# Kernel optimization log

Hardware: AMD Instinct MI355X
Metric: run time of the kernel (lower is better)

## Reference

```python
import jax, jax.numpy as jnp
import numpy as np

D_MODEL = 2048
N_EXPERTS = 64
TOP_K = 8
N_TOKENS = 16384


def setup_inputs() -> dict:
    key = jax.random.key(0)
    k1, k2 = jax.random.split(key)
    x_flat = jax.random.normal(k1, (N_TOKENS, D_MODEL), dtype=jnp.float32)
    # nn.Linear(d_model, n_experts) weight has shape [n_experts, d_model]
    gate_w = jax.random.normal(k2, (N_EXPERTS, D_MODEL), dtype=jnp.float32) * (1.0 / np.sqrt(D_MODEL))
    return {"x_flat": x_flat, "gate_w": gate_w}


def reference(x_flat, gate_w):
    # logits = x_flat @ gate_w.T : [tokens, n_experts]
    logits = jnp.einsum("td,ed->te", x_flat, gate_w)
    full_probs = jax.nn.softmax(logits, axis=-1)
    topk_logits, topk_idx = jax.lax.top_k(logits, TOP_K)
    topk_weights = jax.nn.softmax(topk_logits, axis=-1)
    return topk_idx, topk_weights, full_probs, logits
```

## Files before the change

### kernel.cpp

```cpp
#include <hip/hip_runtime.h>
#include <math.h>

#define D_MODEL   2048
#define N_EXPERTS 64
#define TOP_K     8
#define N_TOKENS  16384
#define TOK_TILE  64
#define NTHREADS  512
#define WS_NEED   (64*4*3*64*16)

typedef __attribute__((ext_vector_type(8))) short bf16x8;
typedef __attribute__((ext_vector_type(4))) float f32x4;
typedef __attribute__((ext_vector_type(4))) int   i32x4;

union FragU { i32x4 i; bf16x8 h; };

__device__ __forceinline__ void split3(float x, unsigned &h, unsigned &m, unsigned &l) {
    unsigned ux = __float_as_uint(x);
    h = ux & 0xffff0000u;
    float mf = x - __uint_as_float(h);
    unsigned um = __float_as_uint(mf) & 0xffff0000u;
    float lf = mf - __uint_as_float(um);
    m = um;
    l = __float_as_uint(lf) & 0xffff0000u;
}

__global__ __launch_bounds__(256) void pack_w_kernel(const float* __restrict__ gw,
                                                     unsigned* __restrict__ wp) {
    const int g    = blockIdx.x * 256 + threadIdx.x;
    const int d    = g & 3;
    const int lane = (g >> 2) & 63;
    const int rest = g >> 8;
    const int v    = rest % 3;
    const int t    = rest / 3;
    const int fr   = t & 3;
    const int ks   = t >> 2;
    const int e    = fr * 16 + (lane & 15);
    const int k    = ks * 32 + (lane >> 4) * 8 + 2 * d;
    const float w0 = gw[(size_t)e * D_MODEL + k];
    const float w1 = gw[(size_t)e * D_MODEL + k + 1];
    unsigned h0, m0, l0, h1, m1, l1;
    split3(w0, h0, m0, l0);
    split3(w1, h1, m1, l1);
    const unsigned c0 = (v == 0) ? h0 : ((v == 1) ? m0 : l0);
    const unsigned c1 = (v == 0) ? h1 : ((v == 1) ? m1 : l1);
    wp[g] = (c0 >> 16) | c1;
}

__device__ __forceinline__ void splitpack(const float4 a, const float4 b,
                                          FragU &ph, FragU &pm, FragU &pl) {
    const float f[8] = {a.x, a.y, a.z, a.w, b.x, b.y, b.z, b.w};
#pragma unroll
    for (int d = 0; d < 4; ++d) {
        unsigned h0, m0, l0, h1, m1, l1;
        split3(f[2 * d],     h0, m0, l0);
        split3(f[2 * d + 1], h1, m1, l1);
        ph.i[d] = (int)((h0 >> 16) | h1);
        pm.i[d] = (int)((m0 >> 16) | m1);
        pl.i[d] = (int)((l0 >> 16) | l1);
    }
}

#define MFMA(A_, B_, C_) C_ = __builtin_amdgcn_mfma_f32_16x16x32_bf16((A_).h, (B_).h, C_, 0, 0, 0)

__global__ __launch_bounds__(NTHREADS) void router_mfma(
    const float* __restrict__ x, const unsigned* __restrict__ wp,
    float* __restrict__ out)
{
    __shared__ float lt[TOK_TILE][N_EXPERTS + 1];
    __shared__ float smax[TOK_TILE], srs[TOK_TILE];

    const int tid  = threadIdx.x;
    const int lane = tid & 63;
    const int wv   = tid >> 6;
    const int mrow = wv & 1;
    const int ncol = (wv >> 1) & 1;
    const int kh   = wv >> 2;
    const int m0   = blockIdx.x * TOK_TILE;

    const int lrow = lane & 15;
    const int lk   = lane >> 4;

    const float* xr0 = x + (size_t)(m0 + mrow * 32 + lrow) * D_MODEL + lk * 8;
    const float* xr1 = xr0 + (size_t)16 * D_MODEL;

    f32x4 acc00 = {0.f, 0.f, 0.f, 0.f};
    f32x4 acc01 = acc00, acc10 = acc00, acc11 = acc00;

    const unsigned* wb = wp + (size_t)(ncol * 2 * 3) * 256 + lane * 4;

    int ks = kh;
    float4 A0a = *(const float4*)(xr0 + ks * 32);
    float4 A0b = *(const float4*)(xr0 + ks * 32 + 4);
    float4 A1a = *(const float4*)(xr1 + ks * 32);
    float4 A1b = *(const float4*)(xr1 + ks * 32 + 4);
    const unsigned* bt = wb + ks * 3072;
    i32x4 B0h = *(const i32x4*)(bt +    0);
    i32x4 B0m = *(const i32x4*)(bt +  256);
    i32x4 B0l = *(const i32x4*)(bt +  512);
    i32x4 B1h = *(const i32x4*)(bt +  768);
    i32x4 B1m = *(const i32x4*)(bt + 1024);
    i32x4 B1l = *(const i32x4*)(bt + 1280);

    auto compute = [&](float4 cA0a, float4 cA0b, float4 cA1a, float4 cA1b,
                       i32x4 cB0h, i32x4 cB0m, i32x4 cB0l,
                       i32x4 cB1h, i32x4 cB1m, i32x4 cB1l) {
        FragU a0h, a0m, a0l, a1h, a1m, a1l;
        splitpack(cA0a, cA0b, a0h, a0m, a0l);
        splitpack(cA1a, cA1b, a1h, a1m, a1l);
        FragU b0h, b0m, b0l, b1h, b1m, b1l;
        b0h.i = cB0h; b0m.i = cB0m; b0l.i = cB0l;
        b1h.i = cB1h; b1m.i = cB1m; b1l.i = cB1l;
        MFMA(a0h, b0h, acc00); MFMA(a0h, b0m, acc00); MFMA(a0m, b0h, acc00);
        MFMA(a0h, b0l, acc00); MFMA(a0l, b0h, acc00); MFMA(a0m, b0m, acc00);
        MFMA(a0h, b1h, acc01); MFMA(a0h, b1m, acc01); MFMA(a0m, b1h, acc01);
        MFMA(a0h, b1l, acc01); MFMA(a0l, b1h, acc01); MFMA(a0m, b1m, acc01);
        MFMA(a1h, b0h, acc10); MFMA(a1h, b0m, acc10); MFMA(a1m, b0h, acc10);
        MFMA(a1h, b0l, acc10); MFMA(a1l, b0h, acc10); MFMA(a1m, b0m, acc10);
        MFMA(a1h, b1h, acc11); MFMA(a1h, b1m, acc11); MFMA(a1m, b1h, acc11);
        MFMA(a1h, b1l, acc11); MFMA(a1l, b1h, acc11); MFMA(a1m, b1m, acc11);
    };

    for (int t = 0; t < 31; ++t) {
        const int ks2 = ks + 2;
        float4 N0a = *(const float4*)(xr0 + ks2 * 32);
        float4 N0b = *(const float4*)(xr0 + ks2 * 32 + 4);
        float4 N1a = *(const float4*)(xr1 + ks2 * 32);
        float4 N1b = *(const float4*)(xr1 + ks2 * 32 + 4);
        const unsigned* bt2 = wb + ks2 * 3072;
        i32x4 C0h = *(const i32x4*)(bt2 +    0);
        i32x4 C0m = *(const i32x4*)(bt2 +  256);
        i32x4 C0l = *(const i32x4*)(bt2 +  512);
        i32x4 C1h = *(const i32x4*)(bt2 +  768);
        i32x4 C1m = *(const i32x4*)(bt2 + 1024);
        i32x4 C1l = *(const i32x4*)(bt2 + 1280);

        compute(A0a, A0b, A1a, A1b, B0h, B0m, B0l, B1h, B1m, B1l);

        A0a = N0a; A0b = N0b; A1a = N1a; A1b = N1b;
        B0h = C0h; B0m = C0m; B0l = C0l; B1h = C1h; B1m = C1m; B1l = C1l;
        ks = ks2;
    }
    compute(A0a, A0b, A1a, A1b, B0h, B0m, B0l, B1h, B1m, B1l);

    if (kh == 1) {
#pragma unroll
        for (int r = 0; r < 4; ++r) {
            lt[mrow * 32 +  0 + lk * 4 + r][ncol * 32 +  0 + lrow] = acc00[r];
            lt[mrow * 32 +  0 + lk * 4 + r][ncol * 32 + 16 + lrow] = acc01[r];
            lt[mrow * 32 + 16 + lk * 4 + r][ncol * 32 +  0 + lrow] = acc10[r];
            lt[mrow * 32 + 16 + lk * 4 + r][ncol * 32 + 16 + lrow] = acc11[r];
        }
    }
    __syncthreads();
    if (kh == 0) {
#pragma unroll
        for (int r = 0; r < 4; ++r) {
            lt[mrow * 32 +  0 + lk * 4 + r][ncol * 32 +  0 + lrow] += acc00[r];
            lt[mrow * 32 +  0 + lk * 4 + r][ncol * 32 + 16 + lrow] += acc01[r];
            lt[mrow * 32 + 16 + lk * 4 + r][ncol * 32 +  0 + lrow] += acc10[r];
            lt[mrow * 32 + 16 + lk * 4 + r][ncol * 32 + 16 + lrow] += acc11[r];
        }
    }
    __syncthreads();

    float* out_idx = out;
    float* out_w   = out + (size_t)N_TOKENS * TOP_K;
    float* out_p   = out + (size_t)2 * N_TOKENS * TOP_K;
    float* out_l   = out_p + (size_t)N_TOKENS * N_EXPERTS;

    if (tid < TOK_TILE) {
        const int t = tid;
        float tv[TOP_K];
        int   ti[TOP_K];
#pragma unroll
        for (int i = 0; i < TOP_K; ++i) { tv[i] = -INFINITY; ti[i] = 0; }
        float m = -INFINITY;

        for (int e = 0; e < N_EXPERTS; ++e) {
            const float v = lt[t][e];
            m = fmaxf(m, v);
            if (v > tv[TOP_K - 1]) {
#pragma unroll
                for (int j = TOP_K - 1; j >= 1; --j) {
                    const bool shift = (v > tv[j - 1]);
                    const bool here  = (v > tv[j]);
                    const float ntv = shift ? tv[j - 1] : (here ? v : tv[j]);
                    const int   nti = shift ? ti[j - 1] : (here ? e : ti[j]);
                    tv[j] = ntv; ti[j] = nti;
                }
                if (v > tv[0]) { tv[0] = v; ti[0] = e; }
            }
        }

        float s = 0.f;
        for (int e = 0; e < N_EXPERTS; ++e) s += expf(lt[t][e] - m);
        const float rs = 1.f / s;
        smax[t] = m;
        srs[t]  = rs;

        float ex[TOP_K];
        float wsum = 0.f;
#pragma unroll
        for (int i = 0; i < TOP_K; ++i) { ex[i] = expf(tv[i] - tv[0]); wsum += ex[i]; }
        const float rw = 1.f / wsum;

        const int tok = m0 + t;
#pragma unroll
        for (int i = 0; i < TOP_K; ++i) {
            out_idx[(size_t)tok * TOP_K + i] = (float)ti[i];
            out_w  [(size_t)tok * TOP_K + i] = ex[i] * rw;
        }
    }
    __syncthreads();

#pragma unroll
    for (int rep = 0; rep < 2; ++rep) {
        const int f = rep * (NTHREADS * 4) + tid * 4;
        const int t = f >> 6;
        const int e = f & 63;
        const float l0 = lt[t][e + 0];
        const float l1 = lt[t][e + 1];
        const float l2 = lt[t][e + 2];
        const float l3 = lt[t][e + 3];
        const float mm = smax[t];
        const float rr = srs[t];
        float4 pv = make_float4(expf(l0 - mm) * rr, expf(l1 - mm) * rr,
                                expf(l2 - mm) * rr, expf(l3 - mm) * rr);
        float4 lv = make_float4(l0, l1, l2, l3);
        const size_t gbase = (size_t)m0 * N_EXPERTS + f;
        *(float4*)(out_p + gbase) = pv;
        *(float4*)(out_l + gbase) = lv;
    }
}

__global__ __launch_bounds__(NTHREADS) void router_fallback(
    const float* __restrict__ x, const float* __restrict__ gw,
    float* __restrict__ out)
{
    __shared__ float xs[TOK_TILE][33];
    __shared__ float wsh[N_EXPERTS][36];
    __shared__ float lt[TOK_TILE][N_EXPERTS + 1];
    __shared__ float smax[TOK_TILE], srs[TOK_TILE];

    const int tid  = threadIdx.x;
    const int lane = tid & 63;
    const int wv   = tid >> 6;
    const int m0   = blockIdx.x * TOK_TILE;
    const int srow = tid >> 3;
    const int skq  = (tid & 7) * 4;

    const float* xsrc = x  + (size_t)(m0 + srow) * D_MODEL + skq;
    const float* wsrc = gw + (size_t)srow        * D_MODEL + skq;
    float4 xr = *(const float4*)(xsrc);
    float4 wr = *(const float4*)(wsrc);

    float acc[8];
#pragma unroll
    for (int i = 0; i < 8; ++i) acc[i] = 0.f;
    const int e0 = wv * 8;

    for (int c = 0; c < D_MODEL / 32; ++c) {
        xs[srow][skq] = xr.x; xs[srow][skq+1] = xr.y; xs[srow][skq+2] = xr.z; xs[srow][skq+3] = xr.w;
        *(float4*)&wsh[srow][skq] = wr;
        __syncthreads();
        if (c + 1 < D_MODEL / 32) {
            xr = *(const float4*)(xsrc + (c + 1) * 32);
            wr = *(const float4*)(wsrc + (c + 1) * 32);
        }
#pragma unroll 8
        for (int k4 = 0; k4 < 8; ++k4) {
            const float4 xv = *(const float4*)&xs[lane][k4 * 4];
#pragma unroll
            for (int e = 0; e < 8; ++e) {
                const float4 w4 = *(const float4*)&wsh[e0 + e][k4 * 4];
                acc[e] = fmaf(xv.x, w4.x, fmaf(xv.y, w4.y, fmaf(xv.z, w4.z, fmaf(xv.w, w4.w, acc[e]))));
            }
        }
        __syncthreads();
    }
#pragma unroll
    for (int e = 0; e < 8; ++e) lt[lane][e0 + e] = acc[e];
    __syncthreads();

    float* out_idx = out;
    float* out_w   = out + (size_t)N_TOKENS * TOP_K;
    float* out_p   = out + (size_t)2 * N_TOKENS * TOP_K;
    float* out_l   = out_p + (size_t)N_TOKENS * N_EXPERTS;

    if (tid < TOK_TILE) {
        const int t = tid;
        float tv[TOP_K]; int ti[TOP_K];
#pragma unroll
        for (int i = 0; i < TOP_K; ++i) { tv[i] = -INFINITY; ti[i] = 0; }
        float m = -INFINITY;
        for (int e = 0; e < N_EXPERTS; ++e) {
            const float v = lt[t][e];
            m = fmaxf(m, v);
            if (v > tv[TOP_K - 1]) {
#pragma unroll
                for (int j = TOP_K - 1; j >= 1; --j) {
                    const bool shift = (v > tv[j - 1]);
                    const bool here  = (v > tv[j]);
                    const float ntv = shift ? tv[j - 1] : (here ? v : tv[j]);
                    const int   nti = shift ? ti[j - 1] : (here ? e : ti[j]);
                    tv[j] = ntv; ti[j] = nti;
                }
                if (v > tv[0]) { tv[0] = v; ti[0] = e; }
            }
        }
        float s = 0.f;
        for (int e = 0; e < N_EXPERTS; ++e) s += expf(lt[t][e] - m);
        const float rs = 1.f / s;
        smax[t] = m; srs[t] = rs;
        float ex[TOP_K]; float wsum = 0.f;
#pragma unroll
        for (int i = 0; i < TOP_K; ++i) { ex[i] = expf(tv[i] - tv[0]); wsum += ex[i]; }
        const float rw = 1.f / wsum;
        const int tok = m0 + t;
#pragma unroll
        for (int i = 0; i < TOP_K; ++i) {
            out_idx[(size_t)tok * TOP_K + i] = (float)ti[i];
            out_w  [(size_t)tok * TOP_K + i] = ex[i] * rw;
        }
    }
    __syncthreads();
#pragma unroll
    for (int rep = 0; rep < 2; ++rep) {
        const int f = rep * (NTHREADS * 4) + tid * 4;
        const int t = f >> 6;
        const int e = f & 63;
        const float l0 = lt[t][e], l1 = lt[t][e+1], l2 = lt[t][e+2], l3 = lt[t][e+3];
        const float mm = smax[t], rr = srs[t];
        float4 pv = make_float4(expf(l0-mm)*rr, expf(l1-mm)*rr, expf(l2-mm)*rr, expf(l3-mm)*rr);
        float4 lv = make_float4(l0, l1, l2, l3);
        const size_t gbase = (size_t)m0 * N_EXPERTS + f;
        *(float4*)(out_p + gbase) = pv;
        *(float4*)(out_l + gbase) = lv;
    }
}

extern "C" void kernel_launch(void* const* d_in, const int* in_sizes, int n_in,
                              void* d_out, int out_size, void* d_ws, size_t ws_size,
                              hipStream_t stream) {
    const float* x  = (const float*)d_in[0];
    const float* gw = (const float*)d_in[1];
    float* out = (float*)d_out;
    if (ws_size >= (size_t)WS_NEED) {
        unsigned* wp = (unsigned*)d_ws;
        pack_w_kernel<<<dim3(WS_NEED / 4 / 256), dim3(256), 0, stream>>>(gw, wp);
        router_mfma<<<dim3(N_TOKENS / TOK_TILE), dim3(NTHREADS), 0, stream>>>(x, wp, out);
    } else {
        router_fallback<<<dim3(N_TOKENS / TOK_TILE), dim3(NTHREADS), 0, stream>>>(x, gw, out);
    }
}
```

Measured before the change: 74.79 us.

## Stage x tiles in swizzled LDS with double buffering, drop K-split across waves

```diff
diff --git a/kernel.cpp b/kernel.cpp
--- a/kernel.cpp
+++ b/kernel.cpp
@@ -67,100 +67,86 @@
     const float* __restrict__ x, const unsigned* __restrict__ wp,
     float* __restrict__ out)
 {
+    __shared__ __align__(16) float xs[2][TOK_TILE][64];
     __shared__ float lt[TOK_TILE][N_EXPERTS + 1];
     __shared__ float smax[TOK_TILE], srs[TOK_TILE];
 
     const int tid  = threadIdx.x;
     const int lane = tid & 63;
     const int wv   = tid >> 6;
-    const int mrow = wv & 1;
-    const int ncol = (wv >> 1) & 1;
-    const int kh   = wv >> 2;
+    const int mrow = wv & 3;
+    const int ncol = wv >> 2;
     const int m0   = blockIdx.x * TOK_TILE;
 
     const int lrow = lane & 15;
     const int lk   = lane >> 4;
 
-    const float* xr0 = x + (size_t)(m0 + mrow * 32 + lrow) * D_MODEL + lk * 8;
-    const float* xr1 = xr0 + (size_t)16 * D_MODEL;
-
-    f32x4 acc00 = {0.f, 0.f, 0.f, 0.f};
-    f32x4 acc01 = acc00, acc10 = acc00, acc11 = acc00;
-
-    const unsigned* wb = wp + (size_t)(ncol * 2 * 3) * 256 + lane * 4;
-
-    int ks = kh;
-    float4 A0a = *(const float4*)(xr0 + ks * 32);
-    float4 A0b = *(const float4*)(xr0 + ks * 32 + 4);
-    float4 A1a = *(const float4*)(xr1 + ks * 32);
-    float4 A1b = *(const float4*)(xr1 + ks * 32 + 4);
-    const unsigned* bt = wb + ks * 3072;
-    i32x4 B0h = *(const i32x4*)(bt +    0);
-    i32x4 B0m = *(const i32x4*)(bt +  256);
-    i32x4 B0l = *(const i32x4*)(bt +  512);
-    i32x4 B1h = *(const i32x4*)(bt +  768);
-    i32x4 B1m = *(const i32x4*)(bt + 1024);
-    i32x4 B1l = *(const i32x4*)(bt + 1280);
-
-    auto compute = [&](float4 cA0a, float4 cA0b, float4 cA1a, float4 cA1b,
-                       i32x4 cB0h, i32x4 cB0m, i32x4 cB0l,
-                       i32x4 cB1h, i32x4 cB1m, i32x4 cB1l) {
-        FragU a0h, a0m, a0l, a1h, a1m, a1l;
-        splitpack(cA0a, cA0b, a0h, a0m, a0l);
-        splitpack(cA1a, cA1b, a1h, a1m, a1l);
-        FragU b0h, b0m, b0l, b1h, b1m, b1l;
-        b0h.i = cB0h; b0m.i = cB0m; b0l.i = cB0l;
-        b1h.i = cB1h; b1m.i = cB1m; b1l.i = cB1l;
-        MFMA(a0h, b0h, acc00); MFMA(a0h, b0m, acc00); MFMA(a0m, b0h, acc00);
-        MFMA(a0h, b0l, acc00); MFMA(a0l, b0h, acc00); MFMA(a0m, b0m, acc00);
-        MFMA(a0h, b1h, acc01); MFMA(a0h, b1m, acc01); MFMA(a0m, b1h, acc01);
-        MFMA(a0h, b1l, acc01); MFMA(a0l, b1h, acc01); MFMA(a0m, b1m, acc01);
-        MFMA(a1h, b0h, acc10); MFMA(a1h, b0m, acc10); MFMA(a1m, b0h, acc10);
-        MFMA(a1h, b0l, acc10); MFMA(a1l, b0h, acc10); MFMA(a1m, b0m, acc10);
-        MFMA(a1h, b1h, acc11); MFMA(a1h, b1m, acc11); MFMA(a1m, b1h, acc11);
-        MFMA(a1h, b1l, acc11); MFMA(a1l, b1h, acc11); MFMA(a1m, b1m, acc11);
-    };
-
-    for (int t = 0; t < 31; ++t) {
-        const int ks2 = ks + 2;
-        float4 N0a = *(const float4*)(xr0 + ks2 * 32);
-        float4 N0b = *(const float4*)(xr0 + ks2 * 32 + 4);
-        float4 N1a = *(const float4*)(xr1 + ks2 * 32);
-        float4 N1b = *(const float4*)(xr1 + ks2 * 32 + 4);
-        const unsigned* bt2 = wb + ks2 * 3072;
-        i32x4 C0h = *(const i32x4*)(bt2 +    0);
-        i32x4 C0m = *(const i32x4*)(bt2 +  256);
-        i32x4 C0l = *(const i32x4*)(bt2 +  512);
-        i32x4 C1h = *(const i32x4*)(bt2 +  768);
-        i32x4 C1m = *(const i32x4*)(bt2 + 1024);
-        i32x4 C1l = *(const i32x4*)(bt2 + 1280);
-
-        compute(A0a, A0b, A1a, A1b, B0h, B0m, B0l, B1h, B1m, B1l);
-
-        A0a = N0a; A0b = N0b; A1a = N1a; A1b = N1b;
-        B0h = C0h; B0m = C0m; B0l = C0l; B1h = C1h; B1m = C1m; B1l = C1l;
-        ks = ks2;
-    }
-    compute(A0a, A0b, A1a, A1b, B0h, B0m, B0l, B1h, B1m, B1l);
-
-    if (kh == 1) {
-#pragma unroll
-        for (int r = 0; r < 4; ++r) {
-            lt[mrow * 32 +  0 + lk * 4 + r][ncol * 32 +  0 + lrow] = acc00[r];
-            lt[mrow * 32 +  0 + lk * 4 + r][ncol * 32 + 16 + lrow] = acc01[r];
-            lt[mrow * 32 + 16 + lk * 4 + r][ncol * 32 +  0 + lrow] = acc10[r];
-            lt[mrow * 32 + 16 + lk * 4 + r][ncol * 32 + 16 + lrow] = acc11[r];
-        }
-    }
-    __syncthreads();
-    if (kh == 0) {
-#pragma unroll
-        for (int r = 0; r < 4; ++r) {
-            lt[mrow * 32 +  0 + lk * 4 + r][ncol * 32 +  0 + lrow] += acc00[r];
-            lt[mrow * 32 +  0 + lk * 4 + r][ncol * 32 + 16 + lrow] += acc01[r];
-            lt[mrow * 32 + 16 + lk * 4 + r][ncol * 32 +  0 + lrow] += acc10[r];
-            lt[mrow * 32 + 16 + lk * 4 + r][ncol * 32 + 16 + lrow] += acc11[r];
-        }
+    const int sr   = tid >> 3;
+    const int s0   = tid & 7;
+    const int wswz = (sr & 7) << 1;
+    float* dstA = &xs[0][sr][4 * (s0 ^ wswz)];
+    float* dstB = &xs[0][sr][4 * ((s0 ^ wswz) ^ 8)];
+    const float* xsrc = x + (size_t)(m0 + sr) * D_MODEL + 4 * s0;
+
+    float4 xa = *(const float4*)(xsrc);
+    float4 xb = *(const float4*)(xsrc + 32);
+    *(float4*)dstA = xa;
+    *(float4*)dstB = xb;
+
+    f32x4 acc0a = {0.f, 0.f, 0.f, 0.f};
+    f32x4 acc0b = acc0a, acc1a = acc0a, acc1b = acc0a;
+
+    const unsigned* wb = wp + (size_t)(ncol * 6) * 256 + lane * 4;
+    const int arow = mrow * 16 + lrow;
+    const int amsk = (lrow & 7) << 1;
+    const int LBUF = TOK_TILE * 64;
+    __syncthreads();
+
+    for (int c = 0; c < 32; ++c) {
+        if (c + 1 < 32) {
+            xa = *(const float4*)(xsrc + (c + 1) * 64);
+            xb = *(const float4*)(xsrc + (c + 1) * 64 + 32);
+        }
+        const float* xbuf = &xs[c & 1][0][0];
+#pragma unroll
+        for (int j = 0; j < 2; ++j) {
+            const int ks = 2 * c + j;
+            const unsigned* bt = wb + (size_t)ks * 3072;
+            i32x4 B0h = *(const i32x4*)(bt +    0);
+            i32x4 B0m = *(const i32x4*)(bt +  256);
+            i32x4 B0l = *(const i32x4*)(bt +  512);
+            i32x4 B1h = *(const i32x4*)(bt +  768);
+            i32x4 B1m = *(const i32x4*)(bt + 1024);
+            i32x4 B1l = *(const i32x4*)(bt + 1280);
+
+            const int slot = (j * 8 + 2 * lk) ^ amsk;
+            const float* ap = xbuf + arow * 64 + 4 * slot;
+            const float4 Aa = *(const float4*)(ap);
+            const float4 Ab = *(const float4*)(ap + 4);
+
+            FragU ah, am, al;
+            splitpack(Aa, Ab, ah, am, al);
+            FragU b0h, b0m, b0l, b1h, b1m, b1l;
+            b0h.i = B0h; b0m.i = B0m; b0l.i = B0l;
+            b1h.i = B1h; b1m.i = B1m; b1l.i = B1l;
+
+            MFMA(ah, b0h, acc0a); MFMA(am, b0h, acc0a); MFMA(al, b0h, acc0a);
+            MFMA(ah, b0m, acc0b); MFMA(am, b0m, acc0b); MFMA(ah, b0l, acc0b);
+            MFMA(ah, b1h, acc1a); MFMA(am, b1h, acc1a); MFMA(al, b1h, acc1a);
+            MFMA(ah, b1m, acc1b); MFMA(am, b1m, acc1b); MFMA(ah, b1l, acc1b);
+        }
+        if (c + 1 < 32) {
+            const int off = ((c + 1) & 1) * LBUF;
+            *(float4*)(dstA + off) = xa;
+            *(float4*)(dstB + off) = xb;
+        }
+        __syncthreads();
+    }
+
+#pragma unroll
+    for (int r = 0; r < 4; ++r) {
+        lt[mrow * 16 + lk * 4 + r][ncol * 32 +  0 + lrow] = acc0a[r] + acc0b[r];
+        lt[mrow * 16 + lk * 4 + r][ncol * 32 + 16 + lrow] = acc1a[r] + acc1b[r];
     }
     __syncthreads();
 
```

Measured after the change: 74.20 us. About the same (-0.8%).

## Split-K router GEMM across many blocks with separate reduce and top-k kernel

Applied to the files above, without the earlier changes.

```diff
diff --git a/kernel.cpp b/kernel.cpp
--- a/kernel.cpp
+++ b/kernel.cpp
@@ -5,9 +5,11 @@
 #define N_EXPERTS 64
 #define TOP_K     8
 #define N_TOKENS  16384
-#define TOK_TILE  64
-#define NTHREADS  512
-#define WS_NEED   (64*4*3*64*16)
+
+#define WS_PACK   786432u
+#define WS_PART   (8u*16384u*64u*4u)
+#define WS_NEED_BIG (WS_PACK + WS_PART)
+#define WS_NEED_MID WS_PACK
 
 typedef __attribute__((ext_vector_type(8))) short bf16x8;
 typedef __attribute__((ext_vector_type(4))) float f32x4;
@@ -63,12 +65,196 @@
 
 #define MFMA(A_, B_, C_) C_ = __builtin_amdgcn_mfma_f32_16x16x32_bf16((A_).h, (B_).h, C_, 0, 0, 0)
 
-__global__ __launch_bounds__(NTHREADS) void router_mfma(
+__global__ __launch_bounds__(512, 4) void gemm_ws(
+    const float* __restrict__ x, const unsigned* __restrict__ wp,
+    float* __restrict__ part)
+{
+    __shared__ __align__(16) float lds[2][64][68];
+
+    const int tid  = threadIdx.x;
+    const int lane = tid & 63;
+    const int w    = tid >> 6;
+    const int eg   = w & 3;
+    const int kg   = w >> 2;
+    const int bx   = blockIdx.x;
+    const int tc   = bx & 255;
+    const int kq   = bx >> 8;
+
+    const int lrow = lane & 15;
+    const int lk   = lane >> 4;
+
+    const int gk0 = kq * 8 + kg * 4;
+    const unsigned* wb = wp + lane * 4;
+#define WOFF(j, p) ((size_t)(((gk0 + (j)) * 4 + eg) * 3 + (p)) * 256)
+    const i32x4 W0h = *(const i32x4*)(wb + WOFF(0,0));
+    const i32x4 W0m = *(const i32x4*)(wb + WOFF(0,1));
+    const i32x4 W0l = *(const i32x4*)(wb + WOFF(0,2));
+    const i32x4 W1h = *(const i32x4*)(wb + WOFF(1,0));
+    const i32x4 W1m = *(const i32x4*)(wb + WOFF(1,1));
+    const i32x4 W1l = *(const i32x4*)(wb + WOFF(1,2));
+    const i32x4 W2h = *(const i32x4*)(wb + WOFF(2,0));
+    const i32x4 W2m = *(const i32x4*)(wb + WOFF(2,1));
+    const i32x4 W2l = *(const i32x4*)(wb + WOFF(2,2));
+    const i32x4 W3h = *(const i32x4*)(wb + WOFF(3,0));
+    const i32x4 W3m = *(const i32x4*)(wb + WOFF(3,1));
+    const i32x4 W3l = *(const i32x4*)(wb + WOFF(3,2));
+#undef WOFF
+
+    const float* pA = x + (size_t)(tc * 64 + lrow) * D_MODEL
+                      + kq * 256 + kg * 128 + lk * 8;
+
+    float4 Ca = *(const float4*)(pA);
+    float4 Cb = *(const float4*)(pA + 4);
+
+    for (int tile = 0; tile < 4; ++tile) {
+        f32x4 accA = {0.f, 0.f, 0.f, 0.f};
+        f32x4 accB = accA;
+
+#define KSTEP(j, WH, WM, WL)                                                 \
+        {                                                                    \
+            const int nt = ((j) < 3) ? tile : tile + 1;                      \
+            const int nj = ((j) + 1) & 3;                                    \
+            float4 Na = Ca, Nb = Cb;                                         \
+            if (!((tile) == 3 && (j) == 3)) {                                \
+                const float* pn = pA + (size_t)nt * 16 * D_MODEL + nj * 32;  \
+                Na = *(const float4*)(pn);                                   \
+                Nb = *(const float4*)(pn + 4);                               \
+            }                                                                \
+            FragU ah, am_, al;                                               \
+            splitpack(Ca, Cb, ah, am_, al);                                  \
+            FragU bh, bm, bl;                                                \
+            bh.i = WH; bm.i = WM; bl.i = WL;                                 \
+            MFMA(ah, bh, accA); MFMA(am_, bh, accA); MFMA(al, bh, accA);     \
+            MFMA(ah, bm, accB); MFMA(am_, bm, accB); MFMA(ah, bl, accB);     \
+            Ca = Na; Cb = Nb;                                                \
+        }
+        KSTEP(0, W0h, W0m, W0l)
+        KSTEP(1, W1h, W1m, W1l)
+        KSTEP(2, W2h, W2m, W2l)
+        KSTEP(3, W3h, W3m, W3l)
+#undef KSTEP
+
+#pragma unroll
+        for (int reg = 0; reg < 4; ++reg)
+            lds[kg][tile * 16 + lk * 4 + reg][eg * 16 + lrow]
+                = accA[reg] + accB[reg];
+    }
+    __syncthreads();
+
+    float* pout = part + (size_t)kq * N_TOKENS * 64 + (size_t)(tc * 64) * 64;
+#pragma unroll
+    for (int it = 0; it < 2; ++it) {
+        const int idx = it * 512 + tid;
+        const int tok = idx >> 4;
+        const int e4  = (idx & 15) * 4;
+        const float4 a = *(const float4*)&lds[0][tok][e4];
+        const float4 b = *(const float4*)&lds[1][tok][e4];
+        float4 r = make_float4(a.x + b.x, a.y + b.y, a.z + b.z, a.w + b.w);
+        *(float4*)(pout + (size_t)tok * 64 + e4) = r;
+    }
+}
+
+__global__ __launch_bounds__(256) void reduce_top(
+    const float* __restrict__ part, float* __restrict__ out)
+{
+    __shared__ float lt[16 * 68 + 32];
+    const int tid = threadIdx.x;
+    const int bx  = blockIdx.x;
+    const int m0  = bx * 16;
+
+    {
+        const int t16 = tid >> 4;
+        const int e4  = (tid & 15) * 4;
+        const size_t tok = (size_t)m0 + t16;
+        float4 s = {0.f, 0.f, 0.f, 0.f};
+#pragma unroll
+        for (int kq = 0; kq < 8; ++kq) {
+            const float4 v = *(const float4*)(part + (size_t)kq * N_TOKENS * 64
+                                              + tok * 64 + e4);
+            s.x += v.x; s.y += v.y; s.z += v.z; s.w += v.w;
+        }
+        *(float4*)(&lt[t16 * 68 + e4]) = s;
+    }
+    __syncthreads();
+
+    float* smax = lt + 16 * 68;
+    float* srs  = smax + 16;
+
+    float* out_idx = out;
+    float* out_w   = out + (size_t)N_TOKENS * TOP_K;
+    float* out_p   = out + (size_t)2 * N_TOKENS * TOP_K;
+    float* out_l   = out_p + (size_t)N_TOKENS * N_EXPERTS;
+
+    if (tid < 16) {
+        const int t = tid;
+        float tv[TOP_K];
+        int   ti[TOP_K];
+#pragma unroll
+        for (int i = 0; i < TOP_K; ++i) { tv[i] = -INFINITY; ti[i] = 0; }
+        float m = -INFINITY;
+
+        for (int e = 0; e < N_EXPERTS; ++e) {
+            const float v = lt[t * 68 + e];
+            m = fmaxf(m, v);
+            if (v > tv[TOP_K - 1]) {
+#pragma unroll
+                for (int j = TOP_K - 1; j >= 1; --j) {
+                    const bool shift = (v > tv[j - 1]);
+                    const bool here  = (v > tv[j]);
+                    const float ntv = shift ? tv[j - 1] : (here ? v : tv[j]);
+                    const int   nti = shift ? ti[j - 1] : (here ? e : ti[j]);
+                    tv[j] = ntv; ti[j] = nti;
+                }
+                if (v > tv[0]) { tv[0] = v; ti[0] = e; }
+            }
+        }
+
+        float s = 0.f;
+        for (int e = 0; e < N_EXPERTS; ++e) s += expf(lt[t * 68 + e] - m);
+        const float rs = 1.f / s;
+        smax[t] = m;
+        srs[t]  = rs;
+
+        float ex[TOP_K];
+        float wsum = 0.f;
+#pragma unroll
+        for (int i = 0; i < TOP_K; ++i) { ex[i] = expf(tv[i] - tv[0]); wsum += ex[i]; }
+        const float rw = 1.f / wsum;
+
+        const int tok = m0 + t;
+#pragma unroll
+        for (int i = 0; i < TOP_K; ++i) {
+            out_idx[(size_t)tok * TOP_K + i] = (float)ti[i];
+            out_w  [(size_t)tok * TOP_K + i] = ex[i] * rw;
+        }
+    }
+    __syncthreads();
+
+    {
+        const int f = tid * 4;
+        const int t = f >> 6;
+        const int e = f & 63;
+        const float l0 = lt[t * 68 + e + 0];
+        const float l1 = lt[t * 68 + e + 1];
+        const float l2 = lt[t * 68 + e + 2];
+        const float l3 = lt[t * 68 + e + 3];
+        const float mm = smax[t];
+        const float rr = srs[t];
+        float4 pv = make_float4(expf(l0 - mm) * rr, expf(l1 - mm) * rr,
+                                expf(l2 - mm) * rr, expf(l3 - mm) * rr);
+        float4 lv = make_float4(l0, l1, l2, l3);
+        const size_t gbase = (size_t)m0 * N_EXPERTS + f;
+        *(float4*)(out_p + gbase) = pv;
+        *(float4*)(out_l + gbase) = lv;
+    }
+}
+
+__global__ __launch_bounds__(512) void router_mfma_mid(
     const float* __restrict__ x, const unsigned* __restrict__ wp,
     float* __restrict__ out)
 {
-    __shared__ float lt[TOK_TILE][N_EXPERTS + 1];
-    __shared__ float smax[TOK_TILE], srs[TOK_TILE];
+    __shared__ float lt[64][N_EXPERTS + 1];
+    __shared__ float smax[64], srs[64];
 
     const int tid  = threadIdx.x;
     const int lane = tid & 63;
@@ -76,7 +262,7 @@
     const int mrow = wv & 1;
     const int ncol = (wv >> 1) & 1;
     const int kh   = wv >> 2;
-    const int m0   = blockIdx.x * TOK_TILE;
+    const int m0   = blockIdx.x * 64;
 
     const int lrow = lane & 15;
     const int lk   = lane >> 4;
@@ -169,14 +355,13 @@
     float* out_p   = out + (size_t)2 * N_TOKENS * TOP_K;
     float* out_l   = out_p + (size_t)N_TOKENS * N_EXPERTS;
 
-    if (tid < TOK_TILE) {
+    if (tid < 64) {
         const int t = tid;
         float tv[TOP_K];
         int   ti[TOP_K];
 #pragma unroll
         for (int i = 0; i < TOP_K; ++i) { tv[i] = -INFINITY; ti[i] = 0; }
         float m = -INFINITY;
-
         for (int e = 0; e < N_EXPERTS; ++e) {
             const float v = lt[t][e];
             m = fmaxf(m, v);
@@ -192,19 +377,14 @@
                 if (v > tv[0]) { tv[0] = v; ti[0] = e; }
             }
         }
-
         float s = 0.f;
         for (int e = 0; e < N_EXPERTS; ++e) s += expf(lt[t][e] - m);
         const float rs = 1.f / s;
-        smax[t] = m;
-        srs[t]  = rs;
-
-        float ex[TOP_K];
-        float wsum = 0.f;
+        smax[t] = m; srs[t] = rs;
+        float ex[TOP_K]; float wsum = 0.f;
 #pragma unroll
         for (int i = 0; i < TOP_K; ++i) { ex[i] = expf(tv[i] - tv[0]); wsum += ex[i]; }
         const float rw = 1.f / wsum;
-
         const int tok = m0 + t;
 #pragma unroll
         for (int i = 0; i < TOP_K; ++i) {
@@ -216,7 +396,7 @@
 
 #pragma unroll
     for (int rep = 0; rep < 2; ++rep) {
-        const int f = rep * (NTHREADS * 4) + tid * 4;
+        const int f = rep * (512 * 4) + tid * 4;
         const int t = f >> 6;
         const int e = f & 63;
         const float l0 = lt[t][e + 0];
@@ -234,19 +414,19 @@
     }
 }
 
-__global__ __launch_bounds__(NTHREADS) void router_fallback(
+__global__ __launch_bounds__(512) void router_fallback(
     const float* __restrict__ x, const float* __restrict__ gw,
     float* __restrict__ out)
 {
-    __shared__ float xs[TOK_TILE][33];
+    __shared__ float xs[64][33];
     __shared__ float wsh[N_EXPERTS][36];
-    __shared__ float lt[TOK_TILE][N_EXPERTS + 1];
-    __shared__ float smax[TOK_TILE], srs[TOK_TILE];
+    __shared__ float lt[64][N_EXPERTS + 1];
+    __shared__ float smax[64], srs[64];
 
     const int tid  = threadIdx.x;
     const int lane = tid & 63;
     const int wv   = tid >> 6;
-    const int m0   = blockIdx.x * TOK_TILE;
+    const int m0   = blockIdx.x * 64;
     const int srow = tid >> 3;
     const int skq  = (tid & 7) * 4;
 
@@ -288,7 +468,7 @@
     float* out_p   = out + (size_t)2 * N_TOKENS * TOP_K;
     float* out_l   = out_p + (size_t)N_TOKENS * N_EXPERTS;
 
-    if (tid < TOK_TILE) {
+    if (tid < 64) {
         const int t = tid;
         float tv[TOP_K]; int ti[TOP_K];
 #pragma unroll
@@ -327,7 +507,7 @@
     __syncthreads();
 #pragma unroll
     for (int rep = 0; rep < 2; ++rep) {
-        const int f = rep * (NTHREADS * 4) + tid * 4;
+        const int f = rep * (512 * 4) + tid * 4;
         const int t = f >> 6;
         const int e = f & 63;
         const float l0 = lt[t][e], l1 = lt[t][e+1], l2 = lt[t][e+2], l3 = lt[t][e+3];
@@ -346,11 +526,17 @@
     const float* x  = (const float*)d_in[0];
     const float* gw = (const float*)d_in[1];
     float* out = (float*)d_out;
-    if (ws_size >= (size_t)WS_NEED) {
+    if (ws_size >= (size_t)WS_NEED_BIG) {
         unsigned* wp = (unsigned*)d_ws;
-        pack_w_kernel<<<dim3(WS_NEED / 4 / 256), dim3(256), 0, stream>>>(gw, wp);
-        router_mfma<<<dim3(N_TOKENS / TOK_TILE), dim3(NTHREADS), 0, stream>>>(x, wp, out);
+        float* part  = (float*)((char*)d_ws + WS_PACK);
+        pack_w_kernel<<<dim3(WS_PACK / 4 / 256), dim3(256), 0, stream>>>(gw, wp);
+        gemm_ws<<<dim3(8 * 256), dim3(512), 0, stream>>>(x, wp, part);
+        reduce_top<<<dim3(N_TOKENS / 16), dim3(256), 0, stream>>>(part, out);
+    } else if (ws_size >= (size_t)WS_NEED_MID) {
+        unsigned* wp = (unsigned*)d_ws;
+        pack_w_kernel<<<dim3(WS_PACK / 4 / 256), dim3(256), 0, stream>>>(gw, wp);
+        router_mfma_mid<<<dim3(N_TOKENS / 64), dim3(512), 0, stream>>>(x, wp, out);
     } else {
-        router_fallback<<<dim3(N_TOKENS / TOK_TILE), dim3(NTHREADS), 0, stream>>>(x, gw, out);
-    }
-}
+        router_fallback<<<dim3(N_TOKENS / 64), dim3(512), 0, stream>>>(x, gw, out);
+    }
+}
```

New measurement: 111.5 us. 49.1% more time.
